# Kernel optimization log

Hardware: AMD Instinct MI355X
Metric: run time of the kernel (lower is better)

Reference implementation:

```python
import jax, jax.numpy as jnp
import numpy as np

N, E, G = 150000, 300000, 4096   # nodes, edges, graphs
H, L = 256, 7                    # hidden_channels, num_gc_layers
ATOM_FEATS, ATOM_VOCAB = 9, 64
BOND_FEATS, BOND_VOCAB = 3, 8
BN_EPS = 1e-5
MSG_EPS = 1e-7


def setup_inputs() -> dict:
    key = jax.random.key(0)
    ks = jax.random.split(key, 10)
    return dict(
        x=jax.random.randint(ks[0], (N, ATOM_FEATS), 0, ATOM_VOCAB),
        edge_index=jax.random.randint(ks[1], (2, E), 0, N),
        edge_attr=jax.random.randint(ks[2], (E, BOND_FEATS), 0, BOND_VOCAB),
        batch=jnp.sort(jax.random.randint(ks[3], (N,), 0, G)),
        atom_emb=jax.random.normal(ks[4], (ATOM_FEATS, ATOM_VOCAB, H), jnp.float32) * 0.02,
        bond_emb=jax.random.normal(ks[5], (BOND_FEATS, BOND_VOCAB, H), jnp.float32) * 0.02,
        vn_weight=jnp.zeros((1, H), jnp.float32),  # Embedding(1,H) init to 0
        conv_w=jax.random.normal(ks[6], (L, H, H), jnp.float32) / np.float32(np.sqrt(H)),
        conv_b=jnp.zeros((L, H), jnp.float32),
        norm_gamma=jnp.ones((L, H), jnp.float32),
        norm_beta=jnp.zeros((L, H), jnp.float32),
        vn_w=jax.random.normal(ks[7], (L - 1, 2, H, H), jnp.float32) / np.float32(np.sqrt(H)),
        vn_b=jnp.zeros((L - 1, 2, H), jnp.float32),
        vn_gamma=jnp.ones((L - 1, 2, H), jnp.float32),
        vn_beta=jnp.zeros((L - 1, 2, H), jnp.float32),
    )


def _bn(x, gamma, beta):
    # BatchNorm1d in training mode (biased batch stats over the node axis)
    mu = jnp.mean(x, axis=0)
    var = jnp.mean(jnp.square(x - mu), axis=0)
    return (x - mu) * jax.lax.rsqrt(var + BN_EPS) * gamma + beta


def _genconv(h, src, dst, edge_emb, w, b):
    # GENConv, aggr='add', mlp_layers=1: msg = relu(x_j + e) + eps; out = Linear(x + sum_agg)
    msg = jax.nn.relu(h[src] + edge_emb) + MSG_EPS            # [E,H]
    agg = jax.ops.segment_sum(msg, dst, num_segments=N)       # [N,H]
    return (h + agg) @ w + b


def reference(x, edge_index, edge_attr, batch, atom_emb, bond_emb, vn_weight,
              conv_w, conv_b, norm_gamma, norm_beta, vn_w, vn_b, vn_gamma, vn_beta):
    src, dst = edge_index[0], edge_index[1]
    # AtomEncoder: sum of per-feature embeddings
    h = jnp.take(atom_emb[0], x[:, 0], axis=0)
    for f in range(1, ATOM_FEATS):
        h = h + jnp.take(atom_emb[f], x[:, f], axis=0)
    # virtual node embedding (one per graph, gathered init from Embedding(1,H))
    vn = jnp.broadcast_to(vn_weight[0], (G, H))
    h = h + vn[batch]
    # BondEncoder (conv_encode_edge=False -> encode once)
    edge_emb = jnp.take(bond_emb[0], edge_attr[:, 0], axis=0)
    for f in range(1, BOND_FEATS):
        edge_emb = edge_emb + jnp.take(bond_emb[f], edge_attr[:, f], axis=0)
    # res+ block: GENConv -> [BN -> ReLU -> VN update -> GENConv -> +res]*
    h = _genconv(h, src, dst, edge_emb, conv_w[0], conv_b[0])
    for layer in range(1, L):
        h2 = jax.nn.relu(_bn(h, norm_gamma[layer - 1], norm_beta[layer - 1]))
        # virtual node: pool + residual, 2-layer MLP (Linear->BN->ReLU twice)
        vn_t = jax.ops.segment_sum(h2, batch, num_segments=G) + vn
        for j in range(2):
            vn_t = jax.nn.relu(_bn(vn_t @ vn_w[layer - 1, j] + vn_b[layer - 1, j],
                                   vn_gamma[layer - 1, j], vn_beta[layer - 1, j]))
        vn = vn_t
        h2 = h2 + vn[batch]
        h = _genconv(h2, src, dst, edge_emb, conv_w[layer], conv_b[layer]) + h
    h = _bn(h, norm_gamma[L - 1], norm_beta[L - 1])
    return jax.ops.segment_sum(h, batch, num_segments=G)  # global_add_pool -> [G,H]
```

## Files before the change

### kernel.cpp

```cpp
#include <hip/hip_runtime.h>
#include <hip/hip_bf16.h>


#define Ncnt 150000
#define Ecnt 300000
#define Gcnt 4096
#define Hc 256
#define Lcnt 7
#define BN_EPS 1e-5f
#define MSG_EPS 1e-7f

typedef __hip_bfloat16 bf16;
typedef __attribute__((ext_vector_type(8))) short bf16x8;
typedef __attribute__((ext_vector_type(8))) unsigned short u16x8;
typedef __attribute__((ext_vector_type(4))) float f32x4;

static __device__ __forceinline__ int imin(int a, int b) { return a < b ? a : b; }

static __device__ __forceinline__ float bs2f(unsigned short s) {
  unsigned u = ((unsigned)s) << 16;
  union { unsigned u; float f; } c; c.u = u; return c.f;
}
static __device__ __forceinline__ unsigned short f2bs(float f) {
  bf16 h = __float2bfloat16(f);
  union { bf16 h; unsigned short s; } c; c.h = h; return c.s;
}
static __device__ __forceinline__ float4 bf4tof4(ushort4 u) {
  float4 r; r.x = bs2f(u.x); r.y = bs2f(u.y); r.z = bs2f(u.z); r.w = bs2f(u.w); return r;
}
static __device__ __forceinline__ ushort4 f4tobf4(float4 v) {
  ushort4 u; u.x = f2bs(v.x); u.y = f2bs(v.y); u.z = f2bs(v.z); u.w = f2bs(v.w); return u;
}

static __device__ __forceinline__ void gll16(const bf16* g, const short* l) {
  __builtin_amdgcn_global_load_lds((const __attribute__((address_space(1))) void*)g,
                                   (__attribute__((address_space(3))) void*)l, 16, 0, 0);
}

__global__ __launch_bounds__(256) void k_zero(float* __restrict__ p, int n) {
  int i = blockIdx.x * 256 + threadIdx.x;
  if (i < n) p[i] = 0.f;
}
__global__ __launch_bounds__(256) void k_zero_int(int* __restrict__ p, int n) {
  int i = blockIdx.x * 256 + threadIdx.x;
  if (i < n) p[i] = 0;
}
__global__ void k_diag(float* __restrict__ out, float v) { out[0] = v; }

__global__ __launch_bounds__(256) void k_bnprep(float* __restrict__ stats,
                                                const float* __restrict__ gamma, const float* __restrict__ beta,
                                                float* __restrict__ scb, float* __restrict__ bbb, float invM) {
  int c = threadIdx.x;
  float mu = stats[c] * invM;
  float var = stats[Hc + c] * invM - mu * mu;
  float sc = rsqrtf(var + BN_EPS) * gamma[c];
  scb[c] = sc;
  bbb[c] = beta[c] - mu * sc;
  stats[c] = 0.f;
  stats[Hc + c] = 0.f;
}

__global__ __launch_bounds__(256) void k_count(const int* __restrict__ ei, int* __restrict__ cnt) {
  int e = blockIdx.x * 256 + threadIdx.x;
  if (e < Ecnt) atomicAdd(&cnt[ei[Ecnt + e]], 1);
}
__global__ __launch_bounds__(256) void k_scan1(const int* __restrict__ cnt, int* __restrict__ rowptr,
                                               int* __restrict__ bsum, int n) {
  __shared__ int sh[256];
  int t = threadIdx.x;
  int i = blockIdx.x * 256 + t;
  int v = (i < n) ? cnt[i] : 0;
  sh[t] = v;
  __syncthreads();
#pragma unroll
  for (int off = 1; off < 256; off <<= 1) {
    int u = (t >= off) ? sh[t - off] : 0;
    __syncthreads();
    sh[t] += u;
    __syncthreads();
  }
  if (i < n) rowptr[i] = sh[t] - v;
  if (t == 255) bsum[blockIdx.x] = sh[255];
}
__global__ __launch_bounds__(1024) void k_scan2(int* __restrict__ bsum, int nb) {
  __shared__ int sh[1024];
  int t = threadIdx.x;
  int v = (t < nb) ? bsum[t] : 0;
  sh[t] = v;
  __syncthreads();
#pragma unroll
  for (int off = 1; off < 1024; off <<= 1) {
    int u = (t >= off) ? sh[t - off] : 0;
    __syncthreads();
    sh[t] += u;
    __syncthreads();
  }
  if (t < nb) bsum[t] = sh[t] - v;
}
__global__ __launch_bounds__(256) void k_scan3(int* __restrict__ rowptr, int* __restrict__ cursor,
                                               const int* __restrict__ bsum, int n) {
  int i = blockIdx.x * 256 + threadIdx.x;
  if (i < n) {
    int v = rowptr[i] + bsum[blockIdx.x];
    rowptr[i] = v;
    cursor[i] = v;
  }
  if (i == 0) rowptr[n] = Ecnt;
}
__global__ __launch_bounds__(256) void k_scatter(const int* __restrict__ ei, const int* __restrict__ ea,
                                                 const int* __restrict__ batch, int* __restrict__ cursor,
                                                 int2* __restrict__ erec) {
  int e = blockIdx.x * 256 + threadIdx.x;
  if (e < Ecnt) {
    int d = ei[Ecnt + e];
    int s = ei[e];
    int packed = ea[e * 3] | (ea[e * 3 + 1] << 3) | (ea[e * 3 + 2] << 6) | (batch[s] << 9);
    int pos = atomicAdd(&cursor[d], 1);
    erec[pos] = make_int2(s, packed);
  }
}

__global__ __launch_bounds__(256) void k_prep_w(const float* __restrict__ W, bf16* __restrict__ hi,
                                                bf16* __restrict__ lo, int nmats) {
  int c = blockIdx.x * 256 + threadIdx.x;
  if (c >= nmats * 8192) return;
  int lane = c & 63;
  int t = c >> 6;
  int kc8 = t & 7;
  int nt = (t >> 3) & 15;
  int m = t >> 7;
  int n = nt * 16 + (lane & 15);
  int k0 = kc8 * 32 + (lane >> 4) * 8;
  bf16x8 hv, lv;
#pragma unroll
  for (int j = 0; j < 8; ++j) {
    float w = W[(size_t)m * 65536 + (size_t)(k0 + j) * 256 + n];
    unsigned short h = f2bs(w);
    float res = w - bs2f(h);
    hv[j] = (short)h;
    lv[j] = (short)f2bs(res);
  }
  *(bf16x8*)&hi[(size_t)c * 8] = hv;
  *(bf16x8*)&lo[(size_t)c * 8] = lv;
}

__global__ __launch_bounds__(256) void k_atom_encode(const int* __restrict__ x,
                                                     const float* __restrict__ aemb,
                                                     const float* __restrict__ vnw,
                                                     bf16* __restrict__ P) {
  int wave = threadIdx.x >> 6, lane = threadIdx.x & 63;
  int r = blockIdx.x * 4 + wave;
  if (r >= Ncnt) return;
  int c4 = lane * 4;
  const int* xr = x + (size_t)r * 9;
  float4 v = *(const float4*)&vnw[c4];
#pragma unroll
  for (int f = 0; f < 9; ++f) {
    float4 e = *(const float4*)&aemb[(size_t)((f << 6) + xr[f]) * Hc + c4];
    v.x += e.x; v.y += e.y; v.z += e.z; v.w += e.w;
  }
  *(ushort4*)&P[(size_t)r * Hc + c4] = f4tobf4(v);
}

__global__ __launch_bounds__(256) void k_init_vn(float* __restrict__ vn, float* __restrict__ vnt,
                                                 const float* __restrict__ vnw) {
  int idx = blockIdx.x * 256 + threadIdx.x;
  float v = vnw[idx & (Hc - 1)];
  vn[idx] = v;
  vnt[idx] = v;
}

__global__ __launch_bounds__(256) void k_agg(const bf16* __restrict__ P, bf16* __restrict__ T,
                                             const int* __restrict__ rowptr, const int2* __restrict__ erec,
                                             const float* __restrict__ bemb,
                                             const float* __restrict__ vn, const int* __restrict__ batch,
                                             const float* __restrict__ scb, const float* __restrict__ bbb) {
  int hw = threadIdx.x >> 5, lane = threadIdx.x & 31;
  int r = blockIdx.x * 8 + hw;
  if (r >= Ncnt) return;
  int c8 = lane * 8;
  bool hasbn = (scb != nullptr);
  float sc[8], bb[8];
  if (hasbn) {
    float4 s0 = *(const float4*)&scb[c8], s1 = *(const float4*)&scb[c8 + 4];
    float4 b0 = *(const float4*)&bbb[c8], b1 = *(const float4*)&bbb[c8 + 4];
    sc[0] = s0.x; sc[1] = s0.y; sc[2] = s0.z; sc[3] = s0.w;
    sc[4] = s1.x; sc[5] = s1.y; sc[6] = s1.z; sc[7] = s1.w;
    bb[0] = b0.x; bb[1] = b0.y; bb[2] = b0.z; bb[3] = b0.w;
    bb[4] = b1.x; bb[5] = b1.y; bb[6] = b1.z; bb[7] = b1.w;
  }
  float acc[8];
  {
    u16x8 pv = *(const u16x8*)&P[(size_t)r * Hc + c8];
    if (hasbn) {
      const float* vr = &vn[(size_t)batch[r] * Hc + c8];
      float4 w0 = *(const float4*)vr, w1 = *(const float4*)(vr + 4);
      float w[8] = {w0.x, w0.y, w0.z, w0.w, w1.x, w1.y, w1.z, w1.w};
#pragma unroll
      for (int k = 0; k < 8; ++k) acc[k] = fmaxf(fmaf(bs2f(pv[k]), sc[k], bb[k]), 0.f) + w[k];
    } else {
#pragma unroll
      for (int k = 0; k < 8; ++k) acc[k] = bs2f(pv[k]);
    }
  }
  int j0 = rowptr[r], j1 = rowptr[r + 1];
  if (j0 < j1) {
    int2 er = erec[j0];
    for (int j = j0; j < j1; ++j) {
      int2 ern = (j + 1 < j1) ? erec[j + 1] : er;
      int s = er.x;
      int a0 = er.y & 7, a1 = (er.y >> 3) & 7, a2 = (er.y >> 6) & 7, g = er.y >> 9;
      u16x8 sv = *(const u16x8*)&P[(size_t)s * Hc + c8];
      const float* e0 = &bemb[(size_t)a0 * Hc + c8];
      const float* e1 = &bemb[(size_t)(8 + a1) * Hc + c8];
      const float* e2 = &bemb[(size_t)(16 + a2) * Hc + c8];
      float4 e0a = *(const float4*)e0, e0b = *(const float4*)(e0 + 4);
      float4 e1a = *(const float4*)e1, e1b = *(const float4*)(e1 + 4);
      float4 e2a = *(const float4*)e2, e2b = *(const float4*)(e2 + 4);
      float em[8] = {e0a.x + e1a.x + e2a.x, e0a.y + e1a.y + e2a.y,
                     e0a.z + e1a.z + e2a.z, e0a.w + e1a.w + e2a.w,
                     e0b.x + e1b.x + e2b.x, e0b.y + e1b.y + e2b.y,
                     e0b.z + e1b.z + e2b.z, e0b.w + e1b.w + e2b.w};
      if (hasbn) {
        const float* vr = &vn[(size_t)g * Hc + c8];
        float4 w0 = *(const float4*)vr, w1 = *(const float4*)(vr + 4);
        float w[8] = {w0.x, w0.y, w0.z, w0.w, w1.x, w1.y, w1.z, w1.w};
#pragma unroll
        for (int k = 0; k < 8; ++k) {
          float v = fmaxf(fmaf(bs2f(sv[k]), sc[k], bb[k]), 0.f) + w[k];
          acc[k] += fmaxf(v + em[k], 0.f) + MSG_EPS;
        }
      } else {
#pragma unroll
        for (int k = 0; k < 8; ++k)
          acc[k] += fmaxf(bs2f(sv[k]) + em[k], 0.f) + MSG_EPS;
      }
      er = ern;
    }
  }
  u16x8 ov;
#pragma unroll
  for (int k = 0; k < 8; ++k) ov[k] = f2bs(acc[k]);
  *(u16x8*)&T[(size_t)r * Hc + c8] = ov;
}

__global__ __launch_bounds__(256) void k_seg_vn(const bf16* __restrict__ P, const int* __restrict__ batch,
                                                float* __restrict__ vnt,
                                                const float* __restrict__ scb, const float* __restrict__ bbb) {
  int wave = threadIdx.x >> 6, lane = threadIdx.x & 63;
  int base = (blockIdx.x * 4 + wave) * 64;
  if (base >= Ncnt) return;
  int c4 = lane * 4;
  float4 scv = *(const float4*)&scb[c4];
  float4 bbv = *(const float4*)&bbb[c4];
  int end = imin(base + 64, Ncnt);
  float4 acc = make_float4(0.f, 0.f, 0.f, 0.f);
  int curg = batch[base];
  for (int r = base; r < end; ++r) {
    int g = batch[r];
    float4 v = bf4tof4(*(const ushort4*)&P[(size_t)r * Hc + c4]);
    v.x = fmaxf(fmaf(v.x, scv.x, bbv.x), 0.f); v.y = fmaxf(fmaf(v.y, scv.y, bbv.y), 0.f);
    v.z = fmaxf(fmaf(v.z, scv.z, bbv.z), 0.f); v.w = fmaxf(fmaf(v.w, scv.w, bbv.w), 0.f);
    if (g != curg) {
      float* d = &vnt[(size_t)curg * Hc + c4];
      atomicAdd(d, acc.x); atomicAdd(d + 1, acc.y); atomicAdd(d + 2, acc.z); atomicAdd(d + 3, acc.w);
      acc = make_float4(0.f, 0.f, 0.f, 0.f);
      curg = g;
    }
    acc.x += v.x; acc.y += v.y; acc.z += v.z; acc.w += v.w;
  }
  float* d = &vnt[(size_t)curg * Hc + c4];
  atomicAdd(d, acc.x); atomicAdd(d + 1, acc.y); atomicAdd(d + 2, acc.z); atomicAdd(d + 3, acc.w);
}

__global__ __launch_bounds__(256) void k_vn_relu(const float* __restrict__ in, float* __restrict__ out,
                                                 float* __restrict__ out2,
                                                 const float* __restrict__ stats,
                                                 const float* __restrict__ gamma, const float* __restrict__ beta,
                                                 float invM) {
  int idx = blockIdx.x * 256 + threadIdx.x;
  int c = idx & (Hc - 1);
  float mu = stats[c] * invM;
  float var = stats[Hc + c] * invM - mu * mu;
  float sc = rsqrtf(var + BN_EPS) * gamma[c];
  float bb = beta[c] - mu * sc;
  float v = fmaxf(fmaf(in[idx], sc, bb), 0.f);
  out[idx] = v;
  out2[idx] = v;
}

__global__ __launch_bounds__(256) void k_bn_pool(const bf16* __restrict__ P, const int* __restrict__ batch,
                                                 float* __restrict__ out,
                                                 const float* __restrict__ scb, const float* __restrict__ bbb) {
  int wave = threadIdx.x >> 6, lane = threadIdx.x & 63;
  int base = (blockIdx.x * 4 + wave) * 64;
  if (base >= Ncnt) return;
  int c4 = lane * 4;
  float4 scv = *(const float4*)&scb[c4];
  float4 bbv = *(const float4*)&bbb[c4];
  int end = imin(base + 64, Ncnt);
  float4 acc = make_float4(0.f, 0.f, 0.f, 0.f);
  int curg = batch[base];
  for (int r = base; r < end; ++r) {
    int g = batch[r];
    float4 v = bf4tof4(*(const ushort4*)&P[(size_t)r * Hc + c4]);
    v.x = fmaf(v.x, scv.x, bbv.x); v.y = fmaf(v.y, scv.y, bbv.y);
    v.z = fmaf(v.z, scv.z, bbv.z); v.w = fmaf(v.w, scv.w, bbv.w);
    if (g != curg) {
      float* d = &out[(size_t)curg * Hc + c4];
      atomicAdd(d, acc.x); atomicAdd(d + 1, acc.y); atomicAdd(d + 2, acc.z); atomicAdd(d + 3, acc.w);
      acc = make_float4(0.f, 0.f, 0.f, 0.f);
      curg = g;
    }
    acc.x += v.x; acc.y += v.y; acc.z += v.z; acc.w += v.w;
  }
  float* d = &out[(size_t)curg * Hc + c4];
  atomicAdd(d, acc.x); atomicAdd(d + 1, acc.y); atomicAdd(d + 2, acc.z); atomicAdd(d + 3, acc.w);
}

__global__ __launch_bounds__(256, 2) void k_gemm_mfma(const bf16* __restrict__ A, const bf16* __restrict__ Whi,
                                                      const bf16* __restrict__ Wlo, const float* __restrict__ bias,
                                                      const bf16* __restrict__ R, bf16* __restrict__ C,
                                                      float* __restrict__ stats, int M) {
  __shared__ __attribute__((aligned(16))) short As[128 * 64];
  __shared__ __attribute__((aligned(16))) unsigned short Cs[32 * 264];
  __shared__ float lsum[256], lsq[256];
  int tid = threadIdx.x;
  int wave = tid >> 6, lane = tid & 63;
  int quad = lane >> 4, l15 = lane & 15;
  int wr = (wave & 1) * 64;
  int wc = (wave >> 1) * 128;
  int row0 = blockIdx.x * 128;

  lsum[tid] = 0.f;
  lsq[tid] = 0.f;

  int sr[4], sjg[4];
#pragma unroll
  for (int i = 0; i < 4; ++i) {
    int s = i * 256 + tid;
    sr[i] = s >> 3;
    sjg[i] = (s & 7) ^ (sr[i] & 7);
  }

  f32x4 acc[4][8];
#pragma unroll
  for (int i = 0; i < 4; ++i)
#pragma unroll
    for (int j = 0; j < 8; ++j) acc[i][j] = (f32x4){0.f, 0.f, 0.f, 0.f};

  for (int kci = 0; kci < 4; ++kci) {
    int kc = kci * 64;
#pragma unroll
    for (int i = 0; i < 4; ++i) {
      int ar = row0 + sr[i]; if (ar >= M) ar = M - 1;
      gll16(A + (size_t)ar * Hc + kc + sjg[i] * 8, &As[(i * 256 + wave * 64) * 8]);
    }
    __syncthreads();
#pragma unroll
    for (int ks = 0; ks < 2; ++ks) {
      int kc8 = kci * 2 + ks;
      int g = ks * 4 + quad;
      bf16x8 af[4];
#pragma unroll
      for (int mi = 0; mi < 4; ++mi) {
        int row = wr + mi * 16 + l15;
        af[mi] = *(const bf16x8*)&As[row * 64 + (g ^ (row & 7)) * 8];
      }
#pragma unroll
      for (int nii = 0; nii < 8; ++nii) {
        int nt = (wave >> 1) * 8 + nii;
        size_t fo = (((size_t)nt * 8 + kc8) * 64 + lane) * 8;
        bf16x8 bh = *(const bf16x8*)&Whi[fo];
        bf16x8 bl = *(const bf16x8*)&Wlo[fo];
#pragma unroll
        for (int mi = 0; mi < 4; ++mi) {
          acc[mi][nii] = __builtin_amdgcn_mfma_f32_16x16x32_bf16(af[mi], bh, acc[mi][nii], 0, 0, 0);
          acc[mi][nii] = __builtin_amdgcn_mfma_f32_16x16x32_bf16(af[mi], bl, acc[mi][nii], 0, 0, 0);
        }
      }
    }
    __syncthreads();
  }

  float s8[8], q8[8];
#pragma unroll
  for (int k = 0; k < 8; ++k) { s8[k] = 0.f; q8[k] = 0.f; }
  int c8 = (tid & 31) * 8;

  for (int p = 0; p < 4; ++p) {
    int lr0 = (wave & 1) * 16 + quad * 4;
#pragma unroll
    for (int ni = 0; ni < 8; ++ni) {
      int col = wc + ni * 16 + l15;
      float bcol = bias[col];
#pragma unroll
      for (int j = 0; j < 4; ++j)
        Cs[(lr0 + j) * 264 + col] = f2bs(acc[p][ni][j] + bcol);
    }
    __syncthreads();
#pragma unroll
    for (int i = 0; i < 4; ++i) {
      int gsl = i * 256 + tid;
      int lr = gsl >> 5;
      int grow = row0 + ((lr < 16) ? p * 16 + lr : 48 + p * 16 + lr);
      if (grow < M) {
        u16x8 cv = *(const u16x8*)&Cs[lr * 264 + c8];
        float v[8];
#pragma unroll
        for (int k = 0; k < 8; ++k) v[k] = bs2f(cv[k]);
        if (R) {
          u16x8 rv = *(const u16x8*)&R[(size_t)grow * Hc + c8];
#pragma unroll
          for (int k = 0; k < 8; ++k) v[k] += bs2f(rv[k]);
        }
        u16x8 ov;
#pragma unroll
        for (int k = 0; k < 8; ++k) {
          ov[k] = f2bs(v[k]);
          s8[k] += v[k];
          q8[k] = fmaf(v[k], v[k], q8[k]);
        }
        *(u16x8*)&C[(size_t)grow * Hc + c8] = ov;
      }
    }
    __syncthreads();
  }

#pragma unroll
  for (int k = 0; k < 8; ++k) {
    atomicAdd(&lsum[c8 + k], s8[k]);
    atomicAdd(&lsq[c8 + k], q8[k]);
  }
  __syncthreads();
  atomicAdd(&stats[tid], lsum[tid]);
  atomicAdd(&stats[Hc + tid], lsq[tid]);
}

__global__ __launch_bounds__(256) void k_gemm_f32(const float* __restrict__ A, const float* __restrict__ W,
                                                  const float* __restrict__ bias, float* __restrict__ C,
                                                  float* __restrict__ statsOut,
                                                  const float* __restrict__ statsIn,
                                                  const float* __restrict__ gIn, const float* __restrict__ bIn,
                                                  float invM, int M) {
  __shared__ float As[64][68];
  __shared__ float Ws[64][68];
  __shared__ float lsum[64], lsq[64];
  int tid = threadIdx.x;
  int row0 = blockIdx.x * 64;
  int col0 = blockIdx.y * 64;
  int tx = tid & 15, ty = tid >> 4;
  if (tid < 64) { lsum[tid] = 0.f; lsq[tid] = 0.f; }
  float acc[4][4] = {{0.f}};
  for (int k0 = 0; k0 < 256; k0 += 64) {
#pragma unroll
    for (int i = 0; i < 4; ++i) {
      int lin = tid + i * 256;
      int r = lin >> 4;
      int c4 = (lin & 15) << 2;
      int gr = row0 + r;
      float4 v = make_float4(0.f, 0.f, 0.f, 0.f);
      if (gr < M) v = *(const float4*)&A[(size_t)gr * Hc + k0 + c4];
      if (statsIn) {
        float4 sv = *(const float4*)&statsIn[k0 + c4];
        float4 qv = *(const float4*)&statsIn[Hc + k0 + c4];
        float4 gv = *(const float4*)&gIn[k0 + c4];
        float4 bv = *(const float4*)&bIn[k0 + c4];
        float mu, var, sc, bb;
        mu = sv.x * invM; var = qv.x * invM - mu * mu; sc = rsqrtf(var + BN_EPS) * gv.x; bb = bv.x - mu * sc;
        v.x = fmaxf(fmaf(v.x, sc, bb), 0.f);
        mu = sv.y * invM; var = qv.y * invM - mu * mu; sc = rsqrtf(var + BN_EPS) * gv.y; bb = bv.y - mu * sc;
        v.y = fmaxf(fmaf(v.y, sc, bb), 0.f);
        mu = sv.z * invM; var = qv.z * invM - mu * mu; sc = rsqrtf(var + BN_EPS) * gv.z; bb = bv.z - mu * sc;
        v.z = fmaxf(fmaf(v.z, sc, bb), 0.f);
        mu = sv.w * invM; var = qv.w * invM - mu * mu; sc = rsqrtf(var + BN_EPS) * gv.w; bb = bv.w - mu * sc;
        v.w = fmaxf(fmaf(v.w, sc, bb), 0.f);
      }
      As[r][c4] = v.x; As[r][c4 + 1] = v.y; As[r][c4 + 2] = v.z; As[r][c4 + 3] = v.w;
      float4 w = *(const float4*)&W[(size_t)(k0 + r) * Hc + col0 + c4];
      Ws[r][c4] = w.x; Ws[r][c4 + 1] = w.y; Ws[r][c4 + 2] = w.z; Ws[r][c4 + 3] = w.w;
    }
    __syncthreads();
#pragma unroll
    for (int k = 0; k < 64; ++k) {
      float a[4], w[4];
#pragma unroll
      for (int i = 0; i < 4; ++i) a[i] = As[ty * 4 + i][k];
#pragma unroll
      for (int j = 0; j < 4; ++j) w[j] = Ws[k][tx * 4 + j];
#pragma unroll
      for (int i = 0; i < 4; ++i)
#pragma unroll
        for (int j = 0; j < 4; ++j) acc[i][j] = fmaf(a[i], w[j], acc[i][j]);
    }
    __syncthreads();
  }
  float cs[4] = {0.f, 0.f, 0.f, 0.f}, cq[4] = {0.f, 0.f, 0.f, 0.f};
#pragma unroll
  for (int i = 0; i < 4; ++i) {
    int gr = row0 + ty * 4 + i;
    if (gr >= M) break;
#pragma unroll
    for (int j = 0; j < 4; ++j) {
      int gc = col0 + tx * 4 + j;
      float v = acc[i][j] + bias[gc];
      C[(size_t)gr * Hc + gc] = v;
      cs[j] += v;
      cq[j] = fmaf(v, v, cq[j]);
    }
  }
#pragma unroll
  for (int j = 0; j < 4; ++j) {
    atomicAdd(&lsum[tx * 4 + j], cs[j]);
    atomicAdd(&lsq[tx * 4 + j], cq[j]);
  }
  __syncthreads();
  if (tid < 64) {
    atomicAdd(&statsOut[col0 + tid], lsum[tid]);
    atomicAdd(&statsOut[Hc + col0 + tid], lsq[tid]);
  }
}

extern "C" void kernel_launch(void* const* d_in, const int* in_sizes, int n_in,
                              void* d_out, int out_size, void* d_ws, size_t ws_size,
                              hipStream_t stream) {
  const int* x = (const int*)d_in[0];
  const int* ei = (const int*)d_in[1];
  const int* ea = (const int*)d_in[2];
  const int* batch = (const int*)d_in[3];
  const float* aemb = (const float*)d_in[4];
  const float* bemb = (const float*)d_in[5];
  const float* vnw = (const float*)d_in[6];
  const float* conv_w = (const float*)d_in[7];
  const float* conv_b = (const float*)d_in[8];
  const float* ngamma = (const float*)d_in[9];
  const float* nbeta = (const float*)d_in[10];
  const float* vn_w = (const float*)d_in[11];
  const float* vn_b = (const float*)d_in[12];
  const float* vn_g = (const float*)d_in[13];
  const float* vn_be = (const float*)d_in[14];
  float* out = (float*)d_out;

  const size_t NODE = (size_t)Ncnt * Hc;
  const size_t GH = (size_t)Gcnt * Hc;
  const int nScanBlk = (Ncnt + 255) / 256;

  size_t off = 0;
  char* base = (char*)d_ws;
  auto take = [&](size_t bytes) { size_t o = off; off += (bytes + 15) & ~(size_t)15; return o; };
  float* vn = (float*)(base + take(GH * 4));
  float* vnt = (float*)(base + take(GH * 4));
  float* vnu = (float*)(base + take(GH * 4));
  float* vnv = (float*)(base + take(GH * 4));
  float* statsN = (float*)(base + take(2 * Hc * 4));
  float* statsV1 = (float*)(base + take(2 * Hc * 4));
  float* statsV2 = (float*)(base + take(2 * Hc * 4));
  float* scbN = (float*)(base + take(Hc * 4));
  float* bbbN = (float*)(base + take(Hc * 4));
  int* rowptr = (int*)(base + take((size_t)(Ncnt + 1) * 4));
  int* cursor = (int*)(base + take((size_t)Ncnt * 4));
  int2* erec = (int2*)(base + take((size_t)Ecnt * 8));
  int* bsum = (int*)(base + take((size_t)nScanBlk * 4));
  bf16* P = (bf16*)(base + take(NODE * 2));
  bf16* T = (bf16*)(base + take(NODE * 2));
  bf16* WhiC = (bf16*)(base + take((size_t)Lcnt * 65536 * 2));
  bf16* WloC = (bf16*)(base + take((size_t)Lcnt * 65536 * 2));
  const size_t NEED = off;
  if (ws_size < NEED) {
    k_zero<<<(int)((GH + 255) / 256), 256, 0, stream>>>(out, (int)GH);
    k_diag<<<1, 1, 0, stream>>>(out, 100000.f + (float)(ws_size / (1024.0 * 1024.0)));
    return;
  }

  const int eBlk = (Ecnt + 255) / 256;
  const int nWaveBlk = (Ncnt + 3) / 4;
  const int aggBlk = (Ncnt + 7) / 8;
  const int segBlk = (Ncnt + 255) / 256;
  const int ggN = (Ncnt + 127) / 128;
  const dim3 gv(Gcnt / 64, 4);
  const float invN = 1.f / Ncnt;
  const float invG = 1.f / Gcnt;

  k_zero_int<<<nScanBlk, 256, 0, stream>>>(cursor, Ncnt);
  k_count<<<eBlk, 256, 0, stream>>>(ei, cursor);
  k_scan1<<<nScanBlk, 256, 0, stream>>>(cursor, rowptr, bsum, Ncnt);
  k_scan2<<<1, 1024, 0, stream>>>(bsum, nScanBlk);
  k_scan3<<<nScanBlk, 256, 0, stream>>>(rowptr, cursor, bsum, Ncnt);
  k_scatter<<<eBlk, 256, 0, stream>>>(ei, ea, batch, cursor, erec);

  k_prep_w<<<(Lcnt * 8192 + 255) / 256, 256, 0, stream>>>(conv_w, WhiC, WloC, Lcnt);

  k_atom_encode<<<nWaveBlk, 256, 0, stream>>>(x, aemb, vnw, P);
  k_init_vn<<<(int)(GH / 256), 256, 0, stream>>>(vn, vnt, vnw);
  k_agg<<<aggBlk, 256, 0, stream>>>(P, T, rowptr, erec, bemb, nullptr, nullptr, nullptr, nullptr);
  k_zero<<<2, 256, 0, stream>>>(statsN, 2 * Hc);
  k_gemm_mfma<<<ggN, 256, 0, stream>>>(T, WhiC, WloC, conv_b, nullptr, P, statsN, Ncnt);

  for (int l = 1; l < Lcnt; ++l) {
    int p = l - 1;
    k_bnprep<<<1, 256, 0, stream>>>(statsN, ngamma + (size_t)p * Hc, nbeta + (size_t)p * Hc,
                                    scbN, bbbN, invN);
    k_seg_vn<<<segBlk, 256, 0, stream>>>(P, batch, vnt, scbN, bbbN);
    k_zero<<<4, 256, 0, stream>>>(statsV1, 4 * Hc);
    k_gemm_f32<<<gv, 256, 0, stream>>>(vnt, vn_w + (size_t)(2 * p) * 65536,
                                       vn_b + (size_t)(2 * p) * Hc, vnu, statsV1,
                                       nullptr, nullptr, nullptr, invG, Gcnt);
    k_gemm_f32<<<gv, 256, 0, stream>>>(vnu, vn_w + (size_t)(2 * p + 1) * 65536,
                                       vn_b + (size_t)(2 * p + 1) * Hc, vnv, statsV2,
                                       statsV1, vn_g + (size_t)(2 * p) * Hc,
                                       vn_be + (size_t)(2 * p) * Hc, invG, Gcnt);
    k_vn_relu<<<(int)(GH / 256), 256, 0, stream>>>(vnv, vn, vnt, statsV2,
                                                   vn_g + (size_t)(2 * p + 1) * Hc,
                                                   vn_be + (size_t)(2 * p + 1) * Hc, invG);
    k_agg<<<aggBlk, 256, 0, stream>>>(P, T, rowptr, erec, bemb, vn, batch, scbN, bbbN);
    k_gemm_mfma<<<ggN, 256, 0, stream>>>(T, WhiC + (size_t)l * 65536, WloC + (size_t)l * 65536,
                                         conv_b + (size_t)l * Hc, P, P, statsN, Ncnt);
  }

  k_bnprep<<<1, 256, 0, stream>>>(statsN, ngamma + (size_t)(Lcnt - 1) * Hc,
                                  nbeta + (size_t)(Lcnt - 1) * Hc, scbN, bbbN, invN);
  k_zero<<<(int)((GH + 255) / 256), 256, 0, stream>>>(out, (int)GH);
  k_bn_pool<<<segBlk, 256, 0, stream>>>(P, batch, out, scbN, bbbN);
}
```

Measured before the change: 2.269 ms.

## Split node GEMM into two column tiles per row block to raise occupancy

```diff
diff --git a/kernel.cpp b/kernel.cpp
--- a/kernel.cpp
+++ b/kernel.cpp
@@ -318,22 +318,22 @@
   atomicAdd(d, acc.x); atomicAdd(d + 1, acc.y); atomicAdd(d + 2, acc.z); atomicAdd(d + 3, acc.w);
 }
 
-__global__ __launch_bounds__(256, 2) void k_gemm_mfma(const bf16* __restrict__ A, const bf16* __restrict__ Whi,
+__global__ __launch_bounds__(256, 3) void k_gemm_mfma(const bf16* __restrict__ A, const bf16* __restrict__ Whi,
                                                       const bf16* __restrict__ Wlo, const float* __restrict__ bias,
                                                       const bf16* __restrict__ R, bf16* __restrict__ C,
                                                       float* __restrict__ stats, int M) {
   __shared__ __attribute__((aligned(16))) short As[128 * 64];
-  __shared__ __attribute__((aligned(16))) unsigned short Cs[32 * 264];
-  __shared__ float lsum[256], lsq[256];
+  __shared__ __attribute__((aligned(16))) unsigned short Cs[32 * 136];
+  __shared__ float lsum[128], lsq[128];
   int tid = threadIdx.x;
   int wave = tid >> 6, lane = tid & 63;
   int quad = lane >> 4, l15 = lane & 15;
   int wr = (wave & 1) * 64;
-  int wc = (wave >> 1) * 128;
-  int row0 = blockIdx.x * 128;
-
-  lsum[tid] = 0.f;
-  lsq[tid] = 0.f;
+  int wc = (wave >> 1) * 64;
+  int c0 = blockIdx.x * 128;
+  int row0 = blockIdx.y * 128;
+
+  if (tid < 128) { lsum[tid] = 0.f; lsq[tid] = 0.f; }
 
   int sr[4], sjg[4];
 #pragma unroll
@@ -343,11 +343,11 @@
     sjg[i] = (s & 7) ^ (sr[i] & 7);
   }
 
-  f32x4 acc[4][8];
+  f32x4 acc[4][4];
 #pragma unroll
   for (int i = 0; i < 4; ++i)
 #pragma unroll
-    for (int j = 0; j < 8; ++j) acc[i][j] = (f32x4){0.f, 0.f, 0.f, 0.f};
+    for (int j = 0; j < 4; ++j) acc[i][j] = (f32x4){0.f, 0.f, 0.f, 0.f};
 
   for (int kci = 0; kci < 4; ++kci) {
     int kc = kci * 64;
@@ -368,8 +368,8 @@
         af[mi] = *(const bf16x8*)&As[row * 64 + (g ^ (row & 7)) * 8];
       }
 #pragma unroll
-      for (int nii = 0; nii < 8; ++nii) {
-        int nt = (wave >> 1) * 8 + nii;
+      for (int nii = 0; nii < 4; ++nii) {
+        int nt = blockIdx.x * 8 + (wave >> 1) * 4 + nii;
         size_t fo = (((size_t)nt * 8 + kc8) * 64 + lane) * 8;
         bf16x8 bh = *(const bf16x8*)&Whi[fo];
         bf16x8 bl = *(const bf16x8*)&Wlo[fo];
@@ -386,31 +386,31 @@
   float s8[8], q8[8];
 #pragma unroll
   for (int k = 0; k < 8; ++k) { s8[k] = 0.f; q8[k] = 0.f; }
-  int c8 = (tid & 31) * 8;
+  int cg8 = (tid & 15) * 8;
 
   for (int p = 0; p < 4; ++p) {
     int lr0 = (wave & 1) * 16 + quad * 4;
 #pragma unroll
-    for (int ni = 0; ni < 8; ++ni) {
+    for (int ni = 0; ni < 4; ++ni) {
       int col = wc + ni * 16 + l15;
-      float bcol = bias[col];
+      float bcol = bias[c0 + col];
 #pragma unroll
       for (int j = 0; j < 4; ++j)
-        Cs[(lr0 + j) * 264 + col] = f2bs(acc[p][ni][j] + bcol);
-    }
-    __syncthreads();
-#pragma unroll
-    for (int i = 0; i < 4; ++i) {
-      int gsl = i * 256 + tid;
-      int lr = gsl >> 5;
-      int grow = row0 + ((lr < 16) ? p * 16 + lr : 48 + p * 16 + lr);
+        Cs[(lr0 + j) * 136 + col] = f2bs(acc[p][ni][j] + bcol);
+    }
+    __syncthreads();
+#pragma unroll
+    for (int i = 0; i < 2; ++i) {
+      int slot = i * 256 + tid;
+      int lr = slot >> 4;
+      int grow = row0 + ((lr < 16) ? p * 16 + lr : 64 + p * 16 + (lr - 16));
       if (grow < M) {
-        u16x8 cv = *(const u16x8*)&Cs[lr * 264 + c8];
+        u16x8 cv = *(const u16x8*)&Cs[lr * 136 + cg8];
         float v[8];
 #pragma unroll
         for (int k = 0; k < 8; ++k) v[k] = bs2f(cv[k]);
         if (R) {
-          u16x8 rv = *(const u16x8*)&R[(size_t)grow * Hc + c8];
+          u16x8 rv = *(const u16x8*)&R[(size_t)grow * Hc + c0 + cg8];
 #pragma unroll
           for (int k = 0; k < 8; ++k) v[k] += bs2f(rv[k]);
         }
@@ -421,7 +421,7 @@
           s8[k] += v[k];
           q8[k] = fmaf(v[k], v[k], q8[k]);
         }
-        *(u16x8*)&C[(size_t)grow * Hc + c8] = ov;
+        *(u16x8*)&C[(size_t)grow * Hc + c0 + cg8] = ov;
       }
     }
     __syncthreads();
@@ -429,12 +429,14 @@
 
 #pragma unroll
   for (int k = 0; k < 8; ++k) {
-    atomicAdd(&lsum[c8 + k], s8[k]);
-    atomicAdd(&lsq[c8 + k], q8[k]);
+    atomicAdd(&lsum[cg8 + k], s8[k]);
+    atomicAdd(&lsq[cg8 + k], q8[k]);
   }
   __syncthreads();
-  atomicAdd(&stats[tid], lsum[tid]);
-  atomicAdd(&stats[Hc + tid], lsq[tid]);
+  if (tid < 128) {
+    atomicAdd(&stats[c0 + tid], lsum[tid]);
+    atomicAdd(&stats[Hc + c0 + tid], lsq[tid]);
+  }
 }
 
 __global__ __launch_bounds__(256) void k_gemm_f32(const float* __restrict__ A, const float* __restrict__ W,
@@ -576,7 +578,7 @@
   const int nWaveBlk = (Ncnt + 3) / 4;
   const int aggBlk = (Ncnt + 7) / 8;
   const int segBlk = (Ncnt + 255) / 256;
-  const int ggN = (Ncnt + 127) / 128;
+  const dim3 ggN(2, (Ncnt + 127) / 128);
   const dim3 gv(Gcnt / 64, 4);
   const float invN = 1.f / Ncnt;
   const float invG = 1.f / Gcnt;
```

After: 2.357 ms. 1.04x slower.
